# Optimization experiments

Hardware: AMD Instinct MI355X
Metric: run time of the kernel (lower is better)

The kernel has to match this reference:

```python
import jax, jax.numpy as jnp
import numpy as np
import math

N, S, E, H = 32, 64, 512, 4
HD = E // H
EQ = E // 4
L2_TEMP = 13.544
LN_EPS = 1e-5


def _ln(x, g, b):
    m = jnp.mean(x, -1, keepdims=True)
    v = jnp.var(x, -1, keepdims=True)
    return (x - m) * jax.lax.rsqrt(v + LN_EPS) * g + b


def setup_inputs() -> dict:
    key = jax.random.key(0)
    ks = jax.random.split(key, 16)
    sc = 0.02
    inp = {
        "x": jax.random.normal(ks[0], (N, S, E), jnp.float32),
        # MultiheadAttention params (torch layout: in_proj_weight (3E,E))
        "Wqkv": jax.random.normal(ks[1], (3 * E, E), jnp.float32) * sc,
        "bqkv": jnp.zeros((3 * E,), jnp.float32),
        "Wo": jax.random.normal(ks[2], (E, E), jnp.float32) * sc,
        "bo": jnp.zeros((E,), jnp.float32),
        # fc1 (E, 2E), fc2 (E, E)
        "W1": jax.random.normal(ks[3], (E, 2 * E), jnp.float32) * sc,
        "b1": jnp.zeros((E,), jnp.float32),
        "W2": jax.random.normal(ks[4], (E, E), jnp.float32) * sc,
        "b2": jnp.zeros((E,), jnp.float32),
        # layer norms
        "g1": jnp.ones((E,), jnp.float32), "be1": jnp.zeros((E,), jnp.float32),
        "g2": jnp.ones((E,), jnp.float32), "be2": jnp.zeros((E,), jnp.float32),
        # fc_diff1: Linear(E, E//4), Linear(E//4, 1)
        "d1W1": jax.random.normal(ks[5], (EQ, E), jnp.float32) * sc,
        "d1b1": jnp.zeros((EQ,), jnp.float32),
        "d1W2": jax.random.normal(ks[6], (1, EQ), jnp.float32) * sc,
        "d1b2": jnp.zeros((1,), jnp.float32),
        # fc_diff2
        "d2W1": jax.random.normal(ks[7], (EQ, E), jnp.float32) * sc,
        "d2b1": jnp.zeros((EQ,), jnp.float32),
        "d2W2": jax.random.normal(ks[8], (1, EQ), jnp.float32) * sc,
        "d2b2": jnp.zeros((1,), jnp.float32),
    }
    return inp


def _mha(x, Wqkv, bqkv, Wo, bo):
    n, s, e = x.shape
    qkv = x @ Wqkv.T + bqkv
    q, k, v = jnp.split(qkv, 3, axis=-1)
    sh = lambda t: t.reshape(n, s, H, HD).transpose(0, 2, 1, 3)  # (n,H,s,hd)
    q, k, v = sh(q), sh(k), sh(v)
    scores = jnp.einsum('bhqd,bhkd->bhqk', q, k) / math.sqrt(HD)
    a = jax.nn.softmax(scores, axis=-1)
    o = jnp.einsum('bhqk,bhkd->bhqd', a, v).transpose(0, 2, 1, 3).reshape(n, s, e)
    return o @ Wo.T + bo, a.mean(axis=1)  # averaged attn weights (torch default)


def _pair_mlp(diff_w, W1a, b1a, W2a, b2a):
    # F.relu applied after every 'layer' (Linear, Dropout(eval=id), Linear)
    h = jax.nn.relu(diff_w @ W1a.T + b1a)  # relu(dropout(relu)) == relu composed -> same
    return jax.nn.relu(h @ W2a.T + b2a)[..., 0]  # (N,f,f)


def reference(x, Wqkv, bqkv, Wo, bo, W1, b1, W2, b2, g1, be1, g2, be2,
              d1W1, d1b1, d1W2, d1b2, d2W1, d2b1, d2W2, d2b2):
    # diff[b,f,g,e] = x[b,g,e] - x[b,f,e]
    diff = x[:, None, :, :] - x[:, :, None, :]  # (N,f,f,E)
    x1_attn = jax.nn.softmax(-jnp.sum(diff * diff, -1) / L2_TEMP, axis=-1)  # (N,f,f)
    x1 = jnp.einsum('bfg,bge->bfe', x1_attn, x)
    x2, x2_attn = _mha(x, Wqkv, bqkv, Wo, bo)
    x_res = jnp.concatenate([x1, x2], axis=-1)
    h = x + jax.nn.relu(x_res @ W1.T + b1)  # dropout eval = identity
    h = _ln(h, g1, be1)
    h = h + jax.nn.relu(h @ W2.T + b2)
    out = _ln(h, g2, be2)
    diff1 = _pair_mlp(diff * x1_attn[..., None], d1W1, d1b1, d1W2, d1b2)
    diff2 = _pair_mlp(diff * x2_attn[..., None], d2W1, d2b1, d2W2, d2b2)
    return out, x1_attn[:, None], x2_attn[:, None], diff1, diff2
```

## Files before the change

kernel.cpp:

```cpp
#include <hip/hip_runtime.h>
#include <math.h>

#define SS 64
#define EE 512
#define L2T 13.544f
#define LNEPS 1e-5f

using bf16x8 = __attribute__((ext_vector_type(8))) __bf16;
using u16x8  = __attribute__((ext_vector_type(8))) unsigned short;
using f32x4  = __attribute__((ext_vector_type(4))) float;

typedef const void __attribute__((address_space(1))) cv_global;
typedef void __attribute__((address_space(3))) v_lds;

__device__ inline unsigned short f2bf(float f) {
    union { float f; unsigned u; } v; v.f = f;
    unsigned r = v.u + 0x7fff + ((v.u >> 16) & 1);
    return (unsigned short)(r >> 16);
}
__device__ inline float bf2f(unsigned short h) {
    union { unsigned u; float f; } v; v.u = (unsigned)h << 16;
    return v.f;
}

#define MFMA16 __builtin_amdgcn_mfma_f32_16x16x32_bf16

#define XB_O    0
#define WFULL_O 1048576
#define W1CB_O  1966080
#define W2B_O   2490368
#define QKVB_O  2752512
#define X1O_O   5898240
#define HB_O    7995392
#define PB_O    9043968

__global__ __launch_bounds__(256)
void mega1(const float* __restrict__ x, const float* __restrict__ Wqkv,
           const float* __restrict__ Wo, const float* __restrict__ W1,
           const float* __restrict__ W2, const float* __restrict__ d1,
           const float* __restrict__ d2, const float* __restrict__ b1,
           const float* __restrict__ bo, unsigned short* __restrict__ bb,
           float* __restrict__ b_eff, float* __restrict__ x1_attn,
           unsigned short* __restrict__ Pl2) {
    const int bx = blockIdx.x, tid = threadIdx.x;
    __shared__ __align__(16) char smem[36096];

    if (bx < 1408) {
        int i = bx * 256 + tid;
        ushort4* dst4 = (ushort4*)bb;
        const float4* s; int di;
        if (i < 196608)      { s = (const float4*)Wqkv + i;          di = WFULL_O/4 + i; }
        else if (i < 212992) { int j = i-196608; s = (const float4*)d1 + j; di = WFULL_O/4 + 196608 + j; }
        else if (i < 229376) { int j = i-212992; s = (const float4*)d2 + j; di = WFULL_O/4 + 212992 + j; }
        else if (i < 294912) { int j = i-229376; s = (const float4*)W2 + j; di = W2B_O/4 + j; }
        else                 { int j = i-294912; int r = j>>7, cq = j&127;
                               s = (const float4*)W1 + r*256 + cq;   di = W1CB_O/4 + r*256 + cq; }
        float4 v = *s;
        ushort4 o;
        o.x = f2bf(v.x); o.y = f2bf(v.y); o.z = f2bf(v.z); o.w = f2bf(v.w);
        dst4[di] = o;
    } else if (bx < 1472) {
        const int tb = bx - 1408;
        const int m0 = (tb >> 3) * 64, n0 = (tb & 7) * 64;
        unsigned short* Asl = (unsigned short*)smem;
        unsigned short* Bsl = Asl + 64 * 40;
        const int wave = tid >> 6, lane = tid & 63;
        const int wm = (wave >> 1) * 32, wn = (wave & 1) * 32;
        const int fr = lane & 15, kq = (lane >> 4) * 8;
        f32x4 acc[2][2] = {};
        for (int k0 = 0; k0 < 512; k0 += 32) {
            {
                int m = tid >> 2, kk = (tid & 3) * 8;
                const float* src = W1 + (size_t)(m0 + m) * 1024 + 512 + k0 + kk;
                float4 v0 = *(const float4*)src, v1 = *(const float4*)(src + 4);
                u16x8 t = {f2bf(v0.x), f2bf(v0.y), f2bf(v0.z), f2bf(v0.w),
                           f2bf(v1.x), f2bf(v1.y), f2bf(v1.z), f2bf(v1.w)};
                *(u16x8*)(Asl + m * 40 + kk) = t;
            }
            {
                int k = tid >> 3, jq = (tid & 7) * 8;
                const float* src = Wo + (size_t)(k0 + k) * 512 + n0 + jq;
                float4 v0 = *(const float4*)src, v1 = *(const float4*)(src + 4);
                float vv[8] = {v0.x, v0.y, v0.z, v0.w, v1.x, v1.y, v1.z, v1.w};
                #pragma unroll
                for (int e = 0; e < 8; ++e) Bsl[(jq + e) * 40 + k] = f2bf(vv[e]);
            }
            __syncthreads();
            bf16x8 a0 = *(const bf16x8*)(Asl + (wm + fr) * 40 + kq);
            bf16x8 a1 = *(const bf16x8*)(Asl + (wm + 16 + fr) * 40 + kq);
            bf16x8 b0 = *(const bf16x8*)(Bsl + (wn + fr) * 40 + kq);
            bf16x8 b1 = *(const bf16x8*)(Bsl + (wn + 16 + fr) * 40 + kq);
            acc[0][0] = MFMA16(a0, b0, acc[0][0], 0, 0, 0);
            acc[0][1] = MFMA16(a0, b1, acc[0][1], 0, 0, 0);
            acc[1][0] = MFMA16(a1, b0, acc[1][0], 0, 0, 0);
            acc[1][1] = MFMA16(a1, b1, acc[1][1], 0, 0, 0);
            __syncthreads();
        }
        unsigned short* W1cb = bb + W1CB_O;
        const int crow = (lane >> 4) * 4, ccol = lane & 15;
        #pragma unroll
        for (int r2 = 0; r2 < 2; ++r2)
            #pragma unroll
            for (int c2 = 0; c2 < 2; ++c2)
                #pragma unroll
                for (int i = 0; i < 4; ++i) {
                    int m = m0 + wm + r2 * 16 + crow + i;
                    int j = n0 + wn + c2 * 16 + ccol;
                    W1cb[(size_t)m * 1024 + 512 + j] = f2bf(acc[r2][c2][i]);
                }
    } else if (bx < 1476) {
        int n = (bx - 1472) * 128 + (tid >> 1);
        int kh = (tid & 1) * 256;
        float s = 0.f;
        for (int k = 0; k < 256; ++k)
            s += W1[(size_t)n * 1024 + 512 + kh + k] * bo[kh + k];
        s += __shfl_xor(s, 1);
        if ((tid & 1) == 0) b_eff[n] = b1[n] + s;
    } else {
        const int idx = bx - 1476;
        const int b = idx >> 1, hf = idx & 1;
        unsigned short* Xhi = (unsigned short*)smem;
        unsigned short* Xlo = Xhi + 64 * 72;
        float* sc    = (float*)(smem + 18432);
        float* norms = (float*)(smem + 27136);
        const int wave = tid >> 6, lane = tid & 63;
        const int fr = lane & 15;
        const int srow = tid >> 2, scq = (tid & 3) * 16;
        const int wmg = hf * 32 + (wave >> 1) * 16;
        const int wn = (wave & 1) * 32;

        f32x4 acc[2] = {};
        float nsq = 0.f;
        const float* xrow = x + (size_t)b * 32768;
        unsigned short* xbg = bb + XB_O + (size_t)b * 32768;

        for (int k0 = 0; k0 < 512; k0 += 64) {
            const float* src = xrow + srow * 512 + k0 + scq;
            u16x8 hi0, hi1, lo0, lo1;
            #pragma unroll
            for (int e = 0; e < 8; ++e) {
                float v = src[e];
                nsq += v * v;
                unsigned short h = f2bf(v);
                hi0[e] = h; lo0[e] = f2bf(v - bf2f(h));
            }
            #pragma unroll
            for (int e = 0; e < 8; ++e) {
                float v = src[8 + e];
                nsq += v * v;
                unsigned short h = f2bf(v);
                hi1[e] = h; lo1[e] = f2bf(v - bf2f(h));
            }
            *(u16x8*)(Xhi + srow * 72 + scq)     = hi0;
            *(u16x8*)(Xhi + srow * 72 + scq + 8) = hi1;
            *(u16x8*)(Xlo + srow * 72 + scq)     = lo0;
            *(u16x8*)(Xlo + srow * 72 + scq + 8) = lo1;
            if (hf == 0) {
                *(u16x8*)(xbg + srow * 512 + k0 + scq)     = hi0;
                *(u16x8*)(xbg + srow * 512 + k0 + scq + 8) = hi1;
            }
            __syncthreads();
            #pragma unroll
            for (int j = 0; j < 2; ++j) {
                int kk = j * 32 + (lane >> 4) * 8;
                bf16x8 ah = *(const bf16x8*)(Xhi + (wmg + fr) * 72 + kk);
                bf16x8 al = *(const bf16x8*)(Xlo + (wmg + fr) * 72 + kk);
                #pragma unroll
                for (int c2 = 0; c2 < 2; ++c2) {
                    bf16x8 bh = *(const bf16x8*)(Xhi + (wn + c2 * 16 + fr) * 72 + kk);
                    bf16x8 bl = *(const bf16x8*)(Xlo + (wn + c2 * 16 + fr) * 72 + kk);
                    acc[c2] = MFMA16(ah, bh, acc[c2], 0, 0, 0);
                    acc[c2] = MFMA16(ah, bl, acc[c2], 0, 0, 0);
                    acc[c2] = MFMA16(al, bh, acc[c2], 0, 0, 0);
                }
            }
            __syncthreads();
        }
        nsq += __shfl_xor(nsq, 1);
        nsq += __shfl_xor(nsq, 2);
        if ((tid & 3) == 0) norms[srow] = nsq;
        const int crow = (lane >> 4) * 4, ccol = lane & 15;
        #pragma unroll
        for (int c2 = 0; c2 < 2; ++c2)
            #pragma unroll
            for (int i = 0; i < 4; ++i)
                sc[(wmg - hf * 32 + crow + i) * 68 + wn + c2 * 16 + ccol] =
                    acc[c2][i];
        __syncthreads();
        #pragma unroll
        for (int i = 0; i < 8; ++i) {
            int lr = wave * 8 + i;
            int f = hf * 32 + lr;
            float nf = norms[f];
            float val = (2.f * sc[lr * 68 + lane] - nf - norms[lane]) * (1.0f / L2T);
            float mx = val;
            #pragma unroll
            for (int m = 32; m; m >>= 1) mx = fmaxf(mx, __shfl_xor(mx, m));
            float e = expf(val - mx);
            float sum = e;
            #pragma unroll
            for (int m = 32; m; m >>= 1) sum += __shfl_xor(sum, m);
            float a = e / sum;
            x1_attn[((size_t)b * 64 + f) * 64 + lane] = a;
            Pl2[((size_t)b * 64 + f) * 64 + lane] = f2bf(a);
        }
    }
}

__global__ __launch_bounds__(256)
void gemm_qkvp(const unsigned short* __restrict__ A,
               const unsigned short* __restrict__ B,
               const float* __restrict__ bias,
               unsigned short* __restrict__ Cq, unsigned short* __restrict__ Cp,
               const unsigned short* __restrict__ Pl2,
               unsigned short* __restrict__ x1o) {
    __shared__ unsigned short qsm[8704];
    const int tid = threadIdx.x, wave = tid >> 6, lane = tid & 63;
    const int fr = lane & 15;
    const int crow = (lane >> 4) * 4, ccol = lane & 15;

    if (blockIdx.x < 28) {
        unsigned short* Asl = qsm;
        unsigned short* Bsl = qsm + 4096;
        const int m0 = blockIdx.y * 64, n0 = blockIdx.x * 64;
        const int wm = (wave >> 1) * 32, wn = (wave & 1) * 32;
        const int kq4 = lane >> 4;
        f32x4 acc[2][2] = {};

        for (int k0 = 0; k0 < 512; k0 += 64) {
            #pragma unroll
            for (int c0 = 0; c0 < 512; c0 += 256) {
                int cc = c0 + tid, r = cc >> 3, q = cc & 7;
                int col = (q ^ (r & 7)) * 8;
                __builtin_amdgcn_global_load_lds(
                    (cv_global*)(A + (size_t)(m0 + r) * 512 + k0 + col),
                    (v_lds*)(Asl + c0 * 8 + wave * 512), 16, 0, 0);
            }
            #pragma unroll
            for (int c0 = 0; c0 < 512; c0 += 256) {
                int cc = c0 + tid, r = cc >> 3, q = cc & 7;
                int col = (q ^ (r & 7)) * 8;
                __builtin_amdgcn_global_load_lds(
                    (cv_global*)(B + (size_t)(n0 + r) * 512 + k0 + col),
                    (v_lds*)(Bsl + c0 * 8 + wave * 512), 16, 0, 0);
            }
            __syncthreads();
            #pragma unroll
            for (int j = 0; j < 2; ++j) {
                int kc = (lane >> 4) + j * 4;
                int rb0 = wn + fr, rb1 = wn + 16 + fr;
                bf16x8 b0 = *(const bf16x8*)(Bsl + rb0 * 64 + (kc ^ (rb0 & 7)) * 8);
                bf16x8 b1 = *(const bf16x8*)(Bsl + rb1 * 64 + (kc ^ (rb1 & 7)) * 8);
                #pragma unroll
                for (int r = 0; r < 2; ++r) {
                    int ra = wm + r * 16 + fr;
                    bf16x8 af = *(const bf16x8*)(Asl + ra * 64 + (kc ^ (ra & 7)) * 8);
                    acc[r][0] = MFMA16(af, b0, acc[r][0], 0, 0, 0);
                    acc[r][1] = MFMA16(af, b1, acc[r][1], 0, 0, 0);
                }
            }
            __syncthreads();
        }

        if (blockIdx.x < 24) {
            float bj0 = bias[n0 + wn + ccol], bj1 = bias[n0 + wn + 16 + ccol];
            #pragma unroll
            for (int r = 0; r < 2; ++r)
                #pragma unroll
                for (int c = 0; c < 2; ++c) {
                    float bj = c ? bj1 : bj0;
                    #pragma unroll
                    for (int i = 0; i < 4; ++i) {
                        size_t m = (size_t)(m0 + wm + r * 16 + crow + i);
                        int n = n0 + wn + c * 16 + ccol;
                        Cq[m * 1536 + n] = f2bf(acc[r][c][i] + bj);
                    }
                }
        } else {
            int p0 = n0 - 1536;
            #pragma unroll
            for (int r = 0; r < 2; ++r)
                #pragma unroll
                for (int c = 0; c < 2; ++c)
                    #pragma unroll
                    for (int i = 0; i < 4; ++i) {
                        size_t m = (size_t)(m0 + wm + r * 16 + crow + i);
                        int n = p0 + wn + c * 16 + ccol;
                        Cp[m * 256 + n] = f2bf(acc[r][c][i]);
                    }
        }
    } else {
        const int e0 = (blockIdx.x - 28) * 64;
        const int b = blockIdx.y;
        unsigned short* Ap = qsm;
        unsigned short* Xt = qsm + 64 * 68;
        {
            int row = tid >> 2, cq2 = (tid & 3) * 16;
            const unsigned short* src = Pl2 + (size_t)b * 4096 + row * 64 + cq2;
            *(u16x8*)(Ap + row * 68 + cq2)     = *(const u16x8*)src;
            *(u16x8*)(Ap + row * 68 + cq2 + 8) = *(const u16x8*)(src + 8);
        }
        {
            int g = tid >> 2, cq2 = (tid & 3) * 16;
            const unsigned short* src = A + (size_t)b * 32768 + g * 512 + e0 + cq2;
            u16x8 v0 = *(const u16x8*)src, v1 = *(const u16x8*)(src + 8);
            #pragma unroll
            for (int e = 0; e < 8; ++e) Xt[(cq2 + e) * 68 + g] = v0[e];
            #pragma unroll
            for (int e = 0; e < 8; ++e) Xt[(cq2 + 8 + e) * 68 + g] = v1[e];
        }
        __syncthreads();
        const int wm2 = wave * 16, kq = (lane >> 4) * 8;
        f32x4 o[4] = {};
        #pragma unroll
        for (int j = 0; j < 2; ++j) {
            int kk = j * 32 + kq;
            bf16x8 a = *(const bf16x8*)(Ap + (wm2 + fr) * 68 + kk);
            #pragma unroll
            for (int t = 0; t < 4; ++t) {
                bf16x8 bv = *(const bf16x8*)(Xt + (t * 16 + fr) * 68 + kk);
                o[t] = MFMA16(a, bv, o[t], 0, 0, 0);
            }
        }
        #pragma unroll
        for (int t = 0; t < 4; ++t)
            #pragma unroll
            for (int i = 0; i < 4; ++i) {
                size_t m = (size_t)b * 64 + wm2 + crow + i;
                x1o[m * 1024 + e0 + t * 16 + ccol] = f2bf(o[t][i]);
            }
    }
}

__global__ __launch_bounds__(256)
void mha_attn(const unsigned short* __restrict__ qkv,
              unsigned short* __restrict__ x1o, float* __restrict__ pws) {
    const int hh = blockIdx.x;
    const int h = hh >> 1, half = hh & 1;
    const int b = blockIdx.y;
    const int tid = threadIdx.x, wave = tid >> 6, lane = tid & 63;

    __shared__ unsigned short Qs[32 * 136];
    __shared__ unsigned short Ks[64 * 136];
    __shared__ unsigned short Vt[128 * 72];
    __shared__ float sc[32 * 68];
    __shared__ unsigned short Pbf[32 * 72];

    const unsigned short* base = qkv + (size_t)b * 64 * 1536;
    {
        int row = tid >> 3, col = (tid & 7) * 16;
        const unsigned short* src = base + (half * 32 + row) * 1536 + h * 128 + col;
        *(u16x8*)(Qs + row * 136 + col)     = *(const u16x8*)(src);
        *(u16x8*)(Qs + row * 136 + col + 8) = *(const u16x8*)(src + 8);
    }
    {
        int row = tid >> 2, col = (tid & 3) * 32;
        const unsigned short* src = base + row * 1536 + 512 + h * 128 + col;
        #pragma unroll
        for (int j = 0; j < 4; ++j)
            *(u16x8*)(Ks + row * 136 + col + j * 8) = *(const u16x8*)(src + j * 8);
    }
    {
        int g = tid >> 2, col = (tid & 3) * 32;
        const unsigned short* src = base + g * 1536 + 1024 + h * 128 + col;
        #pragma unroll
        for (int j = 0; j < 4; ++j) {
            u16x8 v = *(const u16x8*)(src + j * 8);
            #pragma unroll
            for (int e = 0; e < 8; ++e)
                Vt[(col + j * 8 + e) * 72 + g] = v[e];
        }
    }
    __syncthreads();

    const int fr = lane & 15, kq = (lane >> 4) * 8;
    const int crow = (lane >> 4) * 4, ccol = lane & 15;
    const int wm = (wave >> 1) * 16;
    {
        const int wn = (wave & 1) * 32;
        f32x4 s0 = {0.f, 0.f, 0.f, 0.f}, s1 = s0;
        #pragma unroll
        for (int k0 = 0; k0 < 128; k0 += 32) {
            bf16x8 a  = *(const bf16x8*)(Qs + (wm + fr) * 136 + k0 + kq);
            bf16x8 b0 = *(const bf16x8*)(Ks + (wn + fr) * 136 + k0 + kq);
            bf16x8 b1 = *(const bf16x8*)(Ks + (wn + 16 + fr) * 136 + k0 + kq);
            s0 = MFMA16(a, b0, s0, 0, 0, 0);
            s1 = MFMA16(a, b1, s1, 0, 0, 0);
        }
        const float scale = 0.08838834764831845f;
        #pragma unroll
        for (int r = 0; r < 4; ++r) {
            sc[(wm + crow + r) * 68 + wn + ccol]      = s0[r] * scale;
            sc[(wm + crow + r) * 68 + wn + 16 + ccol] = s1[r] * scale;
        }
    }
    __syncthreads();

    #pragma unroll
    for (int i = 0; i < 8; ++i) {
        int f = wave * 8 + i;
        float v = sc[f * 68 + lane];
        float mx = v;
        #pragma unroll
        for (int m = 32; m; m >>= 1) mx = fmaxf(mx, __shfl_xor(mx, m));
        float e = expf(v - mx);
        float sum = e;
        #pragma unroll
        for (int m = 32; m; m >>= 1) sum += __shfl_xor(sum, m);
        float a = e / sum;
        Pbf[f * 72 + lane] = f2bf(a);
        pws[(((size_t)b * 4 + h) * 64 + half * 32 + f) * 64 + lane] = a;
    }
    __syncthreads();

    {
        const int wn2 = (wave & 1) * 64;
        f32x4 o[4];
        #pragma unroll
        for (int t = 0; t < 4; ++t) o[t] = f32x4{0.f, 0.f, 0.f, 0.f};
        #pragma unroll
        for (int k0 = 0; k0 < 64; k0 += 32) {
            bf16x8 a = *(const bf16x8*)(Pbf + (wm + fr) * 72 + k0 + kq);
            #pragma unroll
            for (int t = 0; t < 4; ++t) {
                bf16x8 bv = *(const bf16x8*)(Vt + (wn2 + t * 16 + fr) * 72 + k0 + kq);
                o[t] = MFMA16(a, bv, o[t], 0, 0, 0);
            }
        }
        #pragma unroll
        for (int t = 0; t < 4; ++t)
            #pragma unroll
            for (int r = 0; r < 4; ++r) {
                size_t m = (size_t)b * 64 + half * 32 + wm + crow + r;
                int col = h * 128 + wn2 + t * 16 + ccol;
                x1o[m * 1024 + 512 + col] = f2bf(o[t][r]);
            }
    }
}

__global__ __launch_bounds__(256)
void w1pair(const unsigned short* __restrict__ x1o,
            const unsigned short* __restrict__ W1cb,
            const float* __restrict__ beff, float* __restrict__ u,
            const unsigned short* __restrict__ Pb,
            const float* __restrict__ a1, const float* __restrict__ pws,
            const float* __restrict__ d1b1, const float* __restrict__ d1w2,
            const float* __restrict__ d1b2, const float* __restrict__ d2b1,
            const float* __restrict__ d2w2, const float* __restrict__ d2b2,
            float* __restrict__ x2_attn, float* __restrict__ out1,
            float* __restrict__ out2) {
    __shared__ unsigned short Asl[32 * 64];
    __shared__ unsigned short Bsl[64 * 64];
    const int bx = blockIdx.x, tid = threadIdx.x;
    const int wave = tid >> 6, lane = tid & 63;

    if (bx < 512) {
        const int m0 = (bx >> 3) * 32, n0 = (bx & 7) * 64;
        const int wm = (wave >> 1) * 16, wn = (wave & 1) * 32;
        const int fr = lane & 15, kq4 = lane >> 4;
        f32x4 acc[2] = {};
        for (int k0 = 0; k0 < 1024; k0 += 64) {
            {
                int r = tid >> 3, q = tid & 7;
                int col = (q ^ (r & 7)) * 8;
                __builtin_amdgcn_global_load_lds(
                    (cv_global*)(x1o + (size_t)(m0 + r) * 1024 + k0 + col),
                    (v_lds*)(Asl + wave * 512), 16, 0, 0);
            }
            #pragma unroll
            for (int c0 = 0; c0 < 512; c0 += 256) {
                int cc = c0 + tid, r = cc >> 3, q = cc & 7;
                int col = (q ^ (r & 7)) * 8;
                __builtin_amdgcn_global_load_lds(
                    (cv_global*)(W1cb + (size_t)(n0 + r) * 1024 + k0 + col),
                    (v_lds*)(Bsl + c0 * 8 + wave * 512), 16, 0, 0);
            }
            __syncthreads();
            #pragma unroll
            for (int j = 0; j < 2; ++j) {
                int kc = kq4 + j * 4;
                int rb0 = wn + fr, rb1 = wn + 16 + fr, ra = wm + fr;
                bf16x8 b0 = *(const bf16x8*)(Bsl + rb0 * 64 + (kc ^ (rb0 & 7)) * 8);
                bf16x8 b1 = *(const bf16x8*)(Bsl + rb1 * 64 + (kc ^ (rb1 & 7)) * 8);
                bf16x8 af = *(const bf16x8*)(Asl + ra * 64 + (kc ^ (ra & 7)) * 8);
                acc[0] = MFMA16(af, b0, acc[0], 0, 0, 0);
                acc[1] = MFMA16(af, b1, acc[1], 0, 0, 0);
            }
            __syncthreads();
        }
        const int crow = (lane >> 4) * 4, ccol = lane & 15;
        #pragma unroll
        for (int c = 0; c < 2; ++c) {
            int n = n0 + wn + c * 16 + ccol;
            float bj = beff[n];
            #pragma unroll
            for (int i = 0; i < 4; ++i) {
                size_t m = (size_t)(m0 + wm + crow + i);
                u[m * 512 + n] = fmaxf(acc[c][i] + bj, 0.f);
            }
        }
    } else {
        const int idx = bx - 512;
        const int f = idx & 63, b = idx >> 6;
        const size_t row = (size_t)b * SS + f;
        const int c0 = lane * 2, c1 = lane * 2 + 1;

        const float p1f0 = bf2f(Pb[row * 256 + c0]),       p1f1 = bf2f(Pb[row * 256 + c1]);
        const float p2f0 = bf2f(Pb[row * 256 + 128 + c0]), p2f1 = bf2f(Pb[row * 256 + 128 + c1]);
        const float w10 = d1w2[c0], w11 = d1w2[c1];
        const float w20 = d2w2[c0], w21 = d2w2[c1];
        const float b10 = d1b1[c0], b11 = d1b1[c1];
        const float b20 = d2b1[c0], b21 = d2b1[c1];
        const float bb1 = d1b2[0], bb2 = d2b2[0];

        const float* a1r = a1 + row * SS;
        const float* ph0 = pws + (((size_t)b * 4 + 0) * 64 + f) * 64;
        const float* ph1 = pws + (((size_t)b * 4 + 1) * 64 + f) * 64;
        const float* ph2 = pws + (((size_t)b * 4 + 2) * 64 + f) * 64;
        const float* ph3 = pws + (((size_t)b * 4 + 3) * 64 + f) * 64;
        const size_t bbase = (size_t)b * SS * 256;

        for (int g = wave; g < 64; g += 4) {
            float aa1 = a1r[g];
            float aa2 = 0.25f * (ph0[g] + ph1[g] + ph2[g] + ph3[g]);
            float q10 = bf2f(Pb[bbase + g * 256 + c0]);
            float q11 = bf2f(Pb[bbase + g * 256 + c1]);
            float q20 = bf2f(Pb[bbase + g * 256 + 128 + c0]);
            float q21 = bf2f(Pb[bbase + g * 256 + 128 + c1]);
            float h10 = fmaxf(aa1 * (q10 - p1f0) + b10, 0.f);
            float h11 = fmaxf(aa1 * (q11 - p1f1) + b11, 0.f);
            float h20 = fmaxf(aa2 * (q20 - p2f0) + b20, 0.f);
            float h21 = fmaxf(aa2 * (q21 - p2f1) + b21, 0.f);
            float s1 = w10 * h10 + w11 * h11;
            float s2 = w20 * h20 + w21 * h21;
            #pragma unroll
            for (int m = 32; m; m >>= 1) {
                s1 += __shfl_xor(s1, m);
                s2 += __shfl_xor(s2, m);
            }
            if (lane == 0) {
                x2_attn[row * SS + g] = aa2;
                out1[row * SS + g] = fmaxf(s1 + bb1, 0.f);
                out2[row * SS + g] = fmaxf(s2 + bb2, 0.f);
            }
        }
    }
}

__global__ __launch_bounds__(256)
void gemm_w2(const unsigned short* __restrict__ A,
             const unsigned short* __restrict__ B,
             const float* __restrict__ bias, float* __restrict__ C) {
    __shared__ unsigned short Asl[32 * 64];
    __shared__ unsigned short Bsl[64 * 64];
    const int tid = threadIdx.x, wave = tid >> 6, lane = tid & 63;
    const int m0 = blockIdx.y * 32, n0 = blockIdx.x * 64;
    const int wm = (wave >> 1) * 16, wn = (wave & 1) * 32;
    const int fr = lane & 15, kq4 = lane >> 4;
    f32x4 acc[2] = {};
    for (int k0 = 0; k0 < 512; k0 += 64) {
        {
            int r = tid >> 3, q = tid & 7;
            int col = (q ^ (r & 7)) * 8;
            __builtin_amdgcn_global_load_lds(
                (cv_global*)(A + (size_t)(m0 + r) * 512 + k0 + col),
                (v_lds*)(Asl + wave * 512), 16, 0, 0);
        }
        #pragma unroll
        for (int c0 = 0; c0 < 512; c0 += 256) {
            int cc = c0 + tid, r = cc >> 3, q = cc & 7;
            int col = (q ^ (r & 7)) * 8;
            __builtin_amdgcn_global_load_lds(
                (cv_global*)(B + (size_t)(n0 + r) * 512 + k0 + col),
                (v_lds*)(Bsl + c0 * 8 + wave * 512), 16, 0, 0);
        }
        __syncthreads();
        #pragma unroll
        for (int j = 0; j < 2; ++j) {
            int kc = kq4 + j * 4;
            int rb0 = wn + fr, rb1 = wn + 16 + fr, ra = wm + fr;
            bf16x8 b0 = *(const bf16x8*)(Bsl + rb0 * 64 + (kc ^ (rb0 & 7)) * 8);
            bf16x8 b1 = *(const bf16x8*)(Bsl + rb1 * 64 + (kc ^ (rb1 & 7)) * 8);
            bf16x8 af = *(const bf16x8*)(Asl + ra * 64 + (kc ^ (ra & 7)) * 8);
            acc[0] = MFMA16(af, b0, acc[0], 0, 0, 0);
            acc[1] = MFMA16(af, b1, acc[1], 0, 0, 0);
        }
        __syncthreads();
    }
    const int crow = (lane >> 4) * 4, ccol = lane & 15;
    #pragma unroll
    for (int c = 0; c < 2; ++c) {
        int n = n0 + wn + c * 16 + ccol;
        float bj = bias[n];
        #pragma unroll
        for (int i = 0; i < 4; ++i) {
            size_t m = (size_t)(m0 + wm + crow + i);
            C[m * 512 + n] = fmaxf(acc[c][i] + bj, 0.f);
        }
    }
}

__global__ __launch_bounds__(256)
void add_ln(const float* __restrict__ base, const float* __restrict__ u,
            const float* __restrict__ gam, const float* __restrict__ bet,
            float* __restrict__ out, unsigned short* __restrict__ outb) {
    const int row = blockIdx.x;
    const int tid = threadIdx.x, wave = tid >> 6, lane = tid & 63;
    const float* br = base + (size_t)row * EE;
    const float* ur = u + (size_t)row * EE;
    float t0 = br[tid] + ur[tid];
    float t1 = br[tid + 256] + ur[tid + 256];
    float s = t0 + t1, sq = t0 * t0 + t1 * t1;
    #pragma unroll
    for (int m = 32; m; m >>= 1) {
        s += __shfl_xor(s, m);
        sq += __shfl_xor(sq, m);
    }
    __shared__ float ssum[4], ssq[4];
    if (lane == 0) { ssum[wave] = s; ssq[wave] = sq; }
    __syncthreads();
    s = ssum[0] + ssum[1] + ssum[2] + ssum[3];
    sq = ssq[0] + ssq[1] + ssq[2] + ssq[3];
    float mean = s * (1.0f / EE);
    float var = sq * (1.0f / EE) - mean * mean;
    float inv = rsqrtf(var + LNEPS);
    float v0 = (t0 - mean) * inv * gam[tid] + bet[tid];
    float v1 = (t1 - mean) * inv * gam[tid + 256] + bet[tid + 256];
    float* orow = out + (size_t)row * EE;
    orow[tid] = v0;
    orow[tid + 256] = v1;
    if (outb) {
        unsigned short* obr = outb + (size_t)row * EE;
        obr[tid] = f2bf(v0);
        obr[tid + 256] = f2bf(v1);
    }
}

extern "C" void kernel_launch(void* const* d_in, const int* in_sizes, int n_in,
                              void* d_out, int out_size, void* d_ws,
                              size_t ws_size, hipStream_t stream) {
    const float* x    = (const float*)d_in[0];
    const float* Wqkv = (const float*)d_in[1];
    const float* bqkv = (const float*)d_in[2];
    const float* Wo   = (const float*)d_in[3];
    const float* bo   = (const float*)d_in[4];
    const float* W1   = (const float*)d_in[5];
    const float* b1   = (const float*)d_in[6];
    const float* W2   = (const float*)d_in[7];
    const float* b2   = (const float*)d_in[8];
    const float* g1   = (const float*)d_in[9];
    const float* be1  = (const float*)d_in[10];
    const float* g2   = (const float*)d_in[11];
    const float* be2  = (const float*)d_in[12];
    const float* d1W1 = (const float*)d_in[13];
    const float* d1b1 = (const float*)d_in[14];
    const float* d1W2 = (const float*)d_in[15];
    const float* d1b2 = (const float*)d_in[16];
    const float* d2W1 = (const float*)d_in[17];
    const float* d2b1 = (const float*)d_in[18];
    const float* d2W2 = (const float*)d_in[19];
    const float* d2b2 = (const float*)d_in[20];

    float* out      = (float*)d_out;
    float* out_main = out;
    float* x1_attn  = out + 1048576;
    float* x2_attn  = out + 1048576 + 131072;
    float* diff1    = out + 1048576 + 2 * 131072;
    float* diff2    = out + 1048576 + 3 * 131072;

    float* ws    = (float*)d_ws;
    float* u_buf = ws;
    float* h_buf = ws + 1048576;
    float* pws   = ws + 2097152;
    float* b_eff = ws + 2621440;
    unsigned short* Pl2 = (unsigned short*)(ws + 2621952);
    unsigned short* bb  = (unsigned short*)(ws + 2687488);

    unsigned short* xb    = bb + XB_O;
    unsigned short* Wfull = bb + WFULL_O;
    unsigned short* W1cb  = bb + W1CB_O;
    unsigned short* W2b   = bb + W2B_O;
    unsigned short* qkvb  = bb + QKVB_O;
    unsigned short* x1o   = bb + X1O_O;
    unsigned short* hb    = bb + HB_O;
    unsigned short* Pb    = bb + PB_O;

    mega1<<<1540, 256, 0, stream>>>(x, Wqkv, Wo, W1, W2, d1W1, d2W1, b1, bo,
                                    bb, b_eff, x1_attn, Pl2);

    gemm_qkvp<<<dim3(36, 32), 256, 0, stream>>>(xb, Wfull, bqkv, qkvb, Pb,
                                                Pl2, x1o);

    mha_attn<<<dim3(8, 32), 256, 0, stream>>>(qkvb, x1o, pws);

    w1pair<<<2560, 256, 0, stream>>>(x1o, W1cb, b_eff, u_buf, Pb, x1_attn, pws,
                                     d1b1, d1W2, d1b2, d2b1, d2W2, d2b2,
                                     x2_attn, diff1, diff2);

    add_ln<<<2048, 256, 0, stream>>>(x, u_buf, g1, be1, h_buf, hb);

    gemm_w2<<<dim3(8, 64), 256, 0, stream>>>(hb, W2b, b2, u_buf);

    add_ln<<<2048, 256, 0, stream>>>(h_buf, u_buf, g2, be2, out_main, nullptr);
}
```

Measured before the change: 176.9 us.

## Move pair-MLP blocks from W1 GEMM kernel into final LayerNorm kernel

The pairwise diff-MLP work moves out of the W1 GEMM launch, which now runs only 512 GEMM blocks, and into the final LayerNorm launch, which grows to 4096 blocks. The aim is to stop the GEMM blocks from queuing behind or contending with the pair work, and to run the pair work alongside the lightweight LayerNorm instead. Separately, the attention kernel now reads the Q fragments straight from global memory rather than staging them in LDS, which removes one LDS copy and reduces shared-memory use. The cost is uncoalesced global reads for Q inside the MFMA loop, and the final kernel becomes heavier.

New measurement: 180.1 us. About the same (+1.8%).

```diff
diff --git a/kernel.cpp b/kernel.cpp
--- a/kernel.cpp
+++ b/kernel.cpp
@@ -224,7 +224,6 @@
         unsigned short* Bsl = qsm + 4096;
         const int m0 = blockIdx.y * 64, n0 = blockIdx.x * 64;
         const int wm = (wave >> 1) * 32, wn = (wave & 1) * 32;
-        const int kq4 = lane >> 4;
         f32x4 acc[2][2] = {};
 
         for (int k0 = 0; k0 < 512; k0 += 64) {
@@ -340,19 +339,12 @@
     const int b = blockIdx.y;
     const int tid = threadIdx.x, wave = tid >> 6, lane = tid & 63;
 
-    __shared__ unsigned short Qs[32 * 136];
     __shared__ unsigned short Ks[64 * 136];
     __shared__ unsigned short Vt[128 * 72];
     __shared__ float sc[32 * 68];
     __shared__ unsigned short Pbf[32 * 72];
 
     const unsigned short* base = qkv + (size_t)b * 64 * 1536;
-    {
-        int row = tid >> 3, col = (tid & 7) * 16;
-        const unsigned short* src = base + (half * 32 + row) * 1536 + h * 128 + col;
-        *(u16x8*)(Qs + row * 136 + col)     = *(const u16x8*)(src);
-        *(u16x8*)(Qs + row * 136 + col + 8) = *(const u16x8*)(src + 8);
-    }
     {
         int row = tid >> 2, col = (tid & 3) * 32;
         const unsigned short* src = base + row * 1536 + 512 + h * 128 + col;
@@ -378,10 +370,12 @@
     const int wm = (wave >> 1) * 16;
     {
         const int wn = (wave & 1) * 32;
+        const unsigned short* qrow =
+            base + (size_t)(half * 32 + wm + fr) * 1536 + h * 128;
         f32x4 s0 = {0.f, 0.f, 0.f, 0.f}, s1 = s0;
         #pragma unroll
         for (int k0 = 0; k0 < 128; k0 += 32) {
-            bf16x8 a  = *(const bf16x8*)(Qs + (wm + fr) * 136 + k0 + kq);
+            bf16x8 a  = *(const bf16x8*)(qrow + k0 + kq);
             bf16x8 b0 = *(const bf16x8*)(Ks + (wn + fr) * 136 + k0 + kq);
             bf16x8 b1 = *(const bf16x8*)(Ks + (wn + 16 + fr) * 136 + k0 + kq);
             s0 = MFMA16(a, b0, s0, 0, 0, 0);
@@ -439,110 +433,55 @@
 }
 
 __global__ __launch_bounds__(256)
-void w1pair(const unsigned short* __restrict__ x1o,
+void w1gemm(const unsigned short* __restrict__ x1o,
             const unsigned short* __restrict__ W1cb,
-            const float* __restrict__ beff, float* __restrict__ u,
-            const unsigned short* __restrict__ Pb,
-            const float* __restrict__ a1, const float* __restrict__ pws,
-            const float* __restrict__ d1b1, const float* __restrict__ d1w2,
-            const float* __restrict__ d1b2, const float* __restrict__ d2b1,
-            const float* __restrict__ d2w2, const float* __restrict__ d2b2,
-            float* __restrict__ x2_attn, float* __restrict__ out1,
-            float* __restrict__ out2) {
+            const float* __restrict__ beff, float* __restrict__ u) {
     __shared__ unsigned short Asl[32 * 64];
     __shared__ unsigned short Bsl[64 * 64];
-    const int bx = blockIdx.x, tid = threadIdx.x;
-    const int wave = tid >> 6, lane = tid & 63;
-
-    if (bx < 512) {
-        const int m0 = (bx >> 3) * 32, n0 = (bx & 7) * 64;
-        const int wm = (wave >> 1) * 16, wn = (wave & 1) * 32;
-        const int fr = lane & 15, kq4 = lane >> 4;
-        f32x4 acc[2] = {};
-        for (int k0 = 0; k0 < 1024; k0 += 64) {
-            {
-                int r = tid >> 3, q = tid & 7;
-                int col = (q ^ (r & 7)) * 8;
-                __builtin_amdgcn_global_load_lds(
-                    (cv_global*)(x1o + (size_t)(m0 + r) * 1024 + k0 + col),
-                    (v_lds*)(Asl + wave * 512), 16, 0, 0);
-            }
-            #pragma unroll
-            for (int c0 = 0; c0 < 512; c0 += 256) {
-                int cc = c0 + tid, r = cc >> 3, q = cc & 7;
-                int col = (q ^ (r & 7)) * 8;
-                __builtin_amdgcn_global_load_lds(
-                    (cv_global*)(W1cb + (size_t)(n0 + r) * 1024 + k0 + col),
-                    (v_lds*)(Bsl + c0 * 8 + wave * 512), 16, 0, 0);
-            }
-            __syncthreads();
-            #pragma unroll
-            for (int j = 0; j < 2; ++j) {
-                int kc = kq4 + j * 4;
-                int rb0 = wn + fr, rb1 = wn + 16 + fr, ra = wm + fr;
-                bf16x8 b0 = *(const bf16x8*)(Bsl + rb0 * 64 + (kc ^ (rb0 & 7)) * 8);
-                bf16x8 b1 = *(const bf16x8*)(Bsl + rb1 * 64 + (kc ^ (rb1 & 7)) * 8);
-                bf16x8 af = *(const bf16x8*)(Asl + ra * 64 + (kc ^ (ra & 7)) * 8);
-                acc[0] = MFMA16(af, b0, acc[0], 0, 0, 0);
-                acc[1] = MFMA16(af, b1, acc[1], 0, 0, 0);
-            }
-            __syncthreads();
-        }
-        const int crow = (lane >> 4) * 4, ccol = lane & 15;
-        #pragma unroll
-        for (int c = 0; c < 2; ++c) {
-            int n = n0 + wn + c * 16 + ccol;
-            float bj = beff[n];
-            #pragma unroll
-            for (int i = 0; i < 4; ++i) {
-                size_t m = (size_t)(m0 + wm + crow + i);
-                u[m * 512 + n] = fmaxf(acc[c][i] + bj, 0.f);
-            }
-        }
-    } else {
-        const int idx = bx - 512;
-        const int f = idx & 63, b = idx >> 6;
-        const size_t row = (size_t)b * SS + f;
-        const int c0 = lane * 2, c1 = lane * 2 + 1;
-
-        const float p1f0 = bf2f(Pb[row * 256 + c0]),       p1f1 = bf2f(Pb[row * 256 + c1]);
-        const float p2f0 = bf2f(Pb[row * 256 + 128 + c0]), p2f1 = bf2f(Pb[row * 256 + 128 + c1]);
-        const float w10 = d1w2[c0], w11 = d1w2[c1];
-        const float w20 = d2w2[c0], w21 = d2w2[c1];
-        const float b10 = d1b1[c0], b11 = d1b1[c1];
-        const float b20 = d2b1[c0], b21 = d2b1[c1];
-        const float bb1 = d1b2[0], bb2 = d2b2[0];
-
-        const float* a1r = a1 + row * SS;
-        const float* ph0 = pws + (((size_t)b * 4 + 0) * 64 + f) * 64;
-        const float* ph1 = pws + (((size_t)b * 4 + 1) * 64 + f) * 64;
-        const float* ph2 = pws + (((size_t)b * 4 + 2) * 64 + f) * 64;
-        const float* ph3 = pws + (((size_t)b * 4 + 3) * 64 + f) * 64;
-        const size_t bbase = (size_t)b * SS * 256;
-
-        for (int g = wave; g < 64; g += 4) {
-            float aa1 = a1r[g];
-            float aa2 = 0.25f * (ph0[g] + ph1[g] + ph2[g] + ph3[g]);
-            float q10 = bf2f(Pb[bbase + g * 256 + c0]);
-            float q11 = bf2f(Pb[bbase + g * 256 + c1]);
-            float q20 = bf2f(Pb[bbase + g * 256 + 128 + c0]);
-            float q21 = bf2f(Pb[bbase + g * 256 + 128 + c1]);
-            float h10 = fmaxf(aa1 * (q10 - p1f0) + b10, 0.f);
-            float h11 = fmaxf(aa1 * (q11 - p1f1) + b11, 0.f);
-            float h20 = fmaxf(aa2 * (q20 - p2f0) + b20, 0.f);
-            float h21 = fmaxf(aa2 * (q21 - p2f1) + b21, 0.f);
-            float s1 = w10 * h10 + w11 * h11;
-            float s2 = w20 * h20 + w21 * h21;
-            #pragma unroll
-            for (int m = 32; m; m >>= 1) {
-                s1 += __shfl_xor(s1, m);
-                s2 += __shfl_xor(s2, m);
-            }
-            if (lane == 0) {
-                x2_attn[row * SS + g] = aa2;
-                out1[row * SS + g] = fmaxf(s1 + bb1, 0.f);
-                out2[row * SS + g] = fmaxf(s2 + bb2, 0.f);
-            }
+    const int tid = threadIdx.x, wave = tid >> 6, lane = tid & 63;
+    const int bx = blockIdx.x;
+    const int m0 = (bx >> 3) * 32, n0 = (bx & 7) * 64;
+    const int wm = (wave >> 1) * 16, wn = (wave & 1) * 32;
+    const int fr = lane & 15, kq4 = lane >> 4;
+    f32x4 acc[2] = {};
+    for (int k0 = 0; k0 < 1024; k0 += 64) {
+        {
+            int r = tid >> 3, q = tid & 7;
+            int col = (q ^ (r & 7)) * 8;
+            __builtin_amdgcn_global_load_lds(
+                (cv_global*)(x1o + (size_t)(m0 + r) * 1024 + k0 + col),
+                (v_lds*)(Asl + wave * 512), 16, 0, 0);
+        }
+        #pragma unroll
+        for (int c0 = 0; c0 < 512; c0 += 256) {
+            int cc = c0 + tid, r = cc >> 3, q = cc & 7;
+            int col = (q ^ (r & 7)) * 8;
+            __builtin_amdgcn_global_load_lds(
+                (cv_global*)(W1cb + (size_t)(n0 + r) * 1024 + k0 + col),
+                (v_lds*)(Bsl + c0 * 8 + wave * 512), 16, 0, 0);
+        }
+        __syncthreads();
+        #pragma unroll
+        for (int j = 0; j < 2; ++j) {
+            int kc = kq4 + j * 4;
+            int rb0 = wn + fr, rb1 = wn + 16 + fr, ra = wm + fr;
+            bf16x8 b0 = *(const bf16x8*)(Bsl + rb0 * 64 + (kc ^ (rb0 & 7)) * 8);
+            bf16x8 b1 = *(const bf16x8*)(Bsl + rb1 * 64 + (kc ^ (rb1 & 7)) * 8);
+            bf16x8 af = *(const bf16x8*)(Asl + ra * 64 + (kc ^ (ra & 7)) * 8);
+            acc[0] = MFMA16(af, b0, acc[0], 0, 0, 0);
+            acc[1] = MFMA16(af, b1, acc[1], 0, 0, 0);
+        }
+        __syncthreads();
+    }
+    const int crow = (lane >> 4) * 4, ccol = lane & 15;
+    #pragma unroll
+    for (int c = 0; c < 2; ++c) {
+        int n = n0 + wn + c * 16 + ccol;
+        float bj = beff[n];
+        #pragma unroll
+        for (int i = 0; i < 4; ++i) {
+            size_t m = (size_t)(m0 + wm + crow + i);
+            u[m * 512 + n] = fmaxf(acc[c][i] + bj, 0.f);
         }
     }
 }
@@ -633,6 +572,91 @@
         unsigned short* obr = outb + (size_t)row * EE;
         obr[tid] = f2bf(v0);
         obr[tid + 256] = f2bf(v1);
+    }
+}
+
+__global__ __launch_bounds__(256)
+void ln2pair(const float* __restrict__ hbuf, const float* __restrict__ u2,
+             const float* __restrict__ gam, const float* __restrict__ bet,
+             float* __restrict__ out,
+             const unsigned short* __restrict__ Pb,
+             const float* __restrict__ a1, const float* __restrict__ pws,
+             const float* __restrict__ d1b1, const float* __restrict__ d1w2,
+             const float* __restrict__ d1b2, const float* __restrict__ d2b1,
+             const float* __restrict__ d2w2, const float* __restrict__ d2b2,
+             float* __restrict__ x2_attn, float* __restrict__ out1,
+             float* __restrict__ out2) {
+    const int bx = blockIdx.x, tid = threadIdx.x;
+    const int wave = tid >> 6, lane = tid & 63;
+    __shared__ float ssum[4], ssq[4];
+
+    if (bx < 2048) {
+        const int row = bx;
+        const float* br = hbuf + (size_t)row * EE;
+        const float* ur = u2 + (size_t)row * EE;
+        float t0 = br[tid] + ur[tid];
+        float t1 = br[tid + 256] + ur[tid + 256];
+        float s = t0 + t1, sq = t0 * t0 + t1 * t1;
+        #pragma unroll
+        for (int m = 32; m; m >>= 1) {
+            s += __shfl_xor(s, m);
+            sq += __shfl_xor(sq, m);
+        }
+        if (lane == 0) { ssum[wave] = s; ssq[wave] = sq; }
+        __syncthreads();
+        s = ssum[0] + ssum[1] + ssum[2] + ssum[3];
+        sq = ssq[0] + ssq[1] + ssq[2] + ssq[3];
+        float mean = s * (1.0f / EE);
+        float var = sq * (1.0f / EE) - mean * mean;
+        float inv = rsqrtf(var + LNEPS);
+        float* orow = out + (size_t)row * EE;
+        orow[tid] = (t0 - mean) * inv * gam[tid] + bet[tid];
+        orow[tid + 256] = (t1 - mean) * inv * gam[tid + 256] + bet[tid + 256];
+    } else {
+        const int idx = bx - 2048;
+        const int f = idx & 63, b = idx >> 6;
+        const size_t row = (size_t)b * SS + f;
+        const int c0 = lane * 2, c1 = lane * 2 + 1;
+
+        const float p1f0 = bf2f(Pb[row * 256 + c0]),       p1f1 = bf2f(Pb[row * 256 + c1]);
+        const float p2f0 = bf2f(Pb[row * 256 + 128 + c0]), p2f1 = bf2f(Pb[row * 256 + 128 + c1]);
+        const float w10 = d1w2[c0], w11 = d1w2[c1];
+        const float w20 = d2w2[c0], w21 = d2w2[c1];
+        const float b10 = d1b1[c0], b11 = d1b1[c1];
+        const float b20 = d2b1[c0], b21 = d2b1[c1];
+        const float bb1 = d1b2[0], bb2 = d2b2[0];
+
+        const float* a1r = a1 + row * SS;
+        const float* ph0 = pws + (((size_t)b * 4 + 0) * 64 + f) * 64;
+        const float* ph1 = pws + (((size_t)b * 4 + 1) * 64 + f) * 64;
+        const float* ph2 = pws + (((size_t)b * 4 + 2) * 64 + f) * 64;
+        const float* ph3 = pws + (((size_t)b * 4 + 3) * 64 + f) * 64;
+        const size_t bbase = (size_t)b * SS * 256;
+
+        for (int g = wave; g < 64; g += 4) {
+            float aa1 = a1r[g];
+            float aa2 = 0.25f * (ph0[g] + ph1[g] + ph2[g] + ph3[g]);
+            float q10 = bf2f(Pb[bbase + g * 256 + c0]);
+            float q11 = bf2f(Pb[bbase + g * 256 + c1]);
+            float q20 = bf2f(Pb[bbase + g * 256 + 128 + c0]);
+            float q21 = bf2f(Pb[bbase + g * 256 + 128 + c1]);
+            float h10 = fmaxf(aa1 * (q10 - p1f0) + b10, 0.f);
+            float h11 = fmaxf(aa1 * (q11 - p1f1) + b11, 0.f);
+            float h20 = fmaxf(aa2 * (q20 - p2f0) + b20, 0.f);
+            float h21 = fmaxf(aa2 * (q21 - p2f1) + b21, 0.f);
+            float s1 = w10 * h10 + w11 * h11;
+            float s2 = w20 * h20 + w21 * h21;
+            #pragma unroll
+            for (int m = 32; m; m >>= 1) {
+                s1 += __shfl_xor(s1, m);
+                s2 += __shfl_xor(s2, m);
+            }
+            if (lane == 0) {
+                x2_attn[row * SS + g] = aa2;
+                out1[row * SS + g] = fmaxf(s1 + bb1, 0.f);
+                out2[row * SS + g] = fmaxf(s2 + bb2, 0.f);
+            }
+        }
     }
 }
 
@@ -693,13 +717,13 @@
 
     mha_attn<<<dim3(8, 32), 256, 0, stream>>>(qkvb, x1o, pws);
 
-    w1pair<<<2560, 256, 0, stream>>>(x1o, W1cb, b_eff, u_buf, Pb, x1_attn, pws,
-                                     d1b1, d1W2, d1b2, d2b1, d2W2, d2b2,
-                                     x2_attn, diff1, diff2);
+    w1gemm<<<512, 256, 0, stream>>>(x1o, W1cb, b_eff, u_buf);
 
     add_ln<<<2048, 256, 0, stream>>>(x, u_buf, g1, be1, h_buf, hb);
 
     gemm_w2<<<dim3(8, 64), 256, 0, stream>>>(hb, W2b, b2, u_buf);
 
-    add_ln<<<2048, 256, 0, stream>>>(h_buf, u_buf, g2, be2, out_main, nullptr);
-}
+    ln2pair<<<4096, 256, 0, stream>>>(h_buf, u_buf, g2, be2, out_main, Pb,
+                                      x1_attn, pws, d1b1, d1W2, d1b2, d2b1,
+                                      d2W2, d2b2, x2_attn, diff1, diff2);
+}
```
